# Kernel optimization log

Measured on AMD Instinct MI355X. Metric: run time of the kernel, lower is better.

The kernel has to match this reference:

```python
import jax, jax.numpy as jnp
import numpy as np

FP8_E4M3_MAX = 448.0  # max finite value of float8_e4m3fn
SCALE = 2.0           # hardcoded activation scale in FP8QDQLinear.__init__
WEIGHT_SCALE = 2.0    # hardcoded weight scale


def quantize_fp8(x, scale):
    # torchao quantize_affine_float8: divide by scale, saturate to fp8 range, cast
    return jnp.clip(x / scale, -FP8_E4M3_MAX, FP8_E4M3_MAX).astype(jnp.float8_e4m3fn)


def dequantize_fp8(q, scale):
    # torchao dequantize_affine_float8: upcast to fp32 then multiply by scale
    return q.astype(jnp.float32) * scale


def setup_inputs() -> dict:
    key = jax.random.key(0)
    k1, k2, k3 = jax.random.split(key, 3)
    in_features, out_features = 4096, 4096
    inp = jax.random.normal(k1, (4, 4096, in_features), dtype=jnp.float32)
    # weight is created as randn().to(float8_e4m3fn) in __init__ (a buffer, not a Parameter)
    weight = jax.random.normal(k2, (out_features, in_features), dtype=jnp.float32).astype(jnp.float8_e4m3fn)
    bias = jax.random.normal(k3, (out_features,), dtype=jnp.float32)
    return {"input": inp, "weight": weight, "bias": bias}


def reference(input, weight, bias):
    # dequantize fp8 weight
    w = dequantize_fp8(weight, WEIGHT_SCALE)            # [O, I] fp32
    # QDQ fake-quant on activations
    dq_input = dequantize_fp8(quantize_fp8(input, SCALE), SCALE)  # [B, S, I]
    # standard linear: y = x @ W^T + b
    out = jnp.einsum('bsi,oi->bso', dq_input, w) + bias
    return out
```

## Files before the change

### kernel.cpp

```cpp
#include <hip/hip_runtime.h>

typedef float f32x4 __attribute__((ext_vector_type(4)));
typedef float f32x16 __attribute__((ext_vector_type(16)));
typedef int i32x4 __attribute__((ext_vector_type(4)));
typedef int i32x8 __attribute__((ext_vector_type(8)));

#define M_DIM 16384L
#define N_DIM 4096L
#define K_DIM 4096L

__device__ __forceinline__ unsigned int f32_to_e4m3(float x, float scale) {
  float v = fminf(fmaxf(x * scale, -448.f), 448.f);
  unsigned int u = __float_as_uint(v);
  unsigned int s = (u >> 24) & 0x80u;
  float ax = fabsf(v);
  unsigned int ua = __float_as_uint(ax);
  unsigned int subn = (unsigned int)rintf(ax * 512.0f);
  unsigned int r = ua + 0x7FFFFu + ((ua >> 20) & 1u);
  unsigned int nrm = ((r >> 20) & 0x7FFu) - 960u;
  unsigned int mag = (ax < 0.015625f) ? subn : nrm;
  return mag | s;
}

__device__ __forceinline__ unsigned int pack4_e4m3(float4 v, float scale) {
  return f32_to_e4m3(v.x, scale) | (f32_to_e4m3(v.y, scale) << 8) |
         (f32_to_e4m3(v.z, scale) << 16) | (f32_to_e4m3(v.w, scale) << 24);
}

__global__ __launch_bounds__(256) void quant_fp8(const float* __restrict__ in,
                                                 unsigned int* __restrict__ out,
                                                 float scale) {
  const long i = (long)blockIdx.x * 256 + threadIdx.x;
  out[i] = pack4_e4m3(reinterpret_cast<const float4*>(in)[i], scale);
}

__device__ __forceinline__ void gld_lds16(const unsigned char* g, unsigned char* l) {
  __builtin_amdgcn_global_load_lds(
      (const __attribute__((address_space(1))) unsigned int*)g,
      (__attribute__((address_space(3))) unsigned int*)l,
      16, 0, 0);
}

__device__ __forceinline__ uint4 quant16(const float* p, float scale) {
  const float4* q = reinterpret_cast<const float4*>(p);
  uint4 r;
  r.x = pack4_e4m3(q[0], scale);
  r.y = pack4_e4m3(q[1], scale);
  r.z = pack4_e4m3(q[2], scale);
  r.w = pack4_e4m3(q[3], scale);
  return r;
}

__device__ __forceinline__ i32x8 ldfrag(const unsigned char* p, int p_lo) {
  i32x4 lo = *reinterpret_cast<const i32x4*>(p + p_lo * 16);
  i32x4 hi = *reinterpret_cast<const i32x4*>(p + (p_lo ^ 1) * 16);
  return i32x8{lo[0], lo[1], lo[2], lo[3], hi[0], hi[1], hi[2], hi[3]};
}

#define MFMA_SC(a, b, c) \
  __builtin_amdgcn_mfma_scale_f32_32x32x64_f8f6f4((a), (b), (c), 0, 0, 0, 0x7F7F7F7F, 0, 0x7F7F7F7F)

#define BARRIER() asm volatile("s_barrier" ::: "memory")

__global__ __launch_bounds__(256, 3) void gemm_fp8_128(
    const unsigned char* __restrict__ A8, const unsigned char* __restrict__ B8,
    const float* __restrict__ bias, float* __restrict__ C) {
  __shared__ unsigned char sA[3 * 8192];
  __shared__ unsigned char sB[3 * 8192];

  const int t = threadIdx.x;
  const int lane = t & 63;
  const int w = t >> 6;
  const int wm = w >> 1;
  const int wn = w & 1;
  const long bx = blockIdx.x;
  const long by = blockIdx.y;

  f32x16 acc[2][2] = {};

  const int l0 = t;
  const int l1 = t + 256;
  const int r0 = l0 >> 2, c0 = (l0 & 3) ^ ((l0 >> 3) & 3);
  const int r1 = l1 >> 2, c1 = (l1 & 3) ^ ((l1 >> 3) & 3);

  const unsigned char* gA0 = A8 + (by * 128 + r0) * K_DIM + c0 * 16 + 128;
  const unsigned char* gA1 = A8 + (by * 128 + r1) * K_DIM + c1 * 16 + 128;
  const unsigned char* gB0 = B8 + (bx * 128 + r0) * K_DIM + c0 * 16 + 128;
  const unsigned char* gB1 = B8 + (bx * 128 + r1) * K_DIM + c1 * 16 + 128;
  const int wofs = w * 1024;

  const int r32 = lane & 31;
  const int key = (lane >> 1) & 3;
  const int p_lo = ((lane >> 5) << 1) ^ key;

  gld_lds16(gA0 - 128, sA + wofs);
  gld_lds16(gA1 - 128, sA + 4096 + wofs);
  gld_lds16(gB0 - 128, sB + wofs);
  gld_lds16(gB1 - 128, sB + 4096 + wofs);
  gld_lds16(gA0 - 64, sA + 8192 + wofs);
  gld_lds16(gA1 - 64, sA + 8192 + 4096 + wofs);
  gld_lds16(gB0 - 64, sB + 8192 + wofs);
  gld_lds16(gB1 - 64, sB + 8192 + 4096 + wofs);
  asm volatile("s_waitcnt vmcnt(4)" ::: "memory");
  BARRIER();

  int b = 0;
  for (int kt = 0; kt < 64; ++kt) {
    int b2 = b + 2;
    if (b2 >= 3) b2 -= 3;
    const bool st = kt < 62;

    if (st) {
      unsigned char* dA = sA + b2 * 8192 + wofs;
      unsigned char* dB = sB + b2 * 8192 + wofs;
      gld_lds16(gA0, dA);
      gld_lds16(gA1, dA + 4096);
      gld_lds16(gB0, dB);
      gld_lds16(gB1, dB + 4096);
      gA0 += 64; gA1 += 64; gB0 += 64; gB1 += 64;
    }

    const unsigned char* sAw = sA + b * 8192 + wm * 4096;
    const unsigned char* sBw = sB + b * 8192 + wn * 4096;
    i32x8 af0 = ldfrag(sAw + r32 * 64, p_lo);
    i32x8 bf0 = ldfrag(sBw + r32 * 64, p_lo);
    i32x8 af1 = ldfrag(sAw + (32 + r32) * 64, p_lo);
    i32x8 bf1 = ldfrag(sBw + (32 + r32) * 64, p_lo);

    __builtin_amdgcn_s_setprio(1);
    acc[0][0] = MFMA_SC(af0, bf0, acc[0][0]);
    acc[0][1] = MFMA_SC(af0, bf1, acc[0][1]);
    acc[1][0] = MFMA_SC(af1, bf0, acc[1][0]);
    acc[1][1] = MFMA_SC(af1, bf1, acc[1][1]);
    __builtin_amdgcn_s_setprio(0);

    if (st) {
      asm volatile("s_waitcnt vmcnt(4)" ::: "memory");
    } else {
      asm volatile("s_waitcnt vmcnt(0)" ::: "memory");
    }
    BARRIER();

    if (++b == 3) b = 0;
  }

  const int mrow = 4 * (lane >> 5);
  const long gm_base = by * 128 + wm * 64;
  const long gn_base = bx * 128 + wn * 64 + r32;
#pragma unroll
  for (int nj = 0; nj < 2; ++nj) {
    const long gn = gn_base + nj * 32;
    const float bv = bias[gn];
#pragma unroll
    for (int mi = 0; mi < 2; ++mi) {
#pragma unroll
      for (int r = 0; r < 16; ++r) {
        const long gm = gm_base + mi * 32 + (r & 3) + 8 * (r >> 2) + mrow;
        C[gm * N_DIM + gn] = acc[mi][nj][r] * 4.0f + bv;
      }
    }
  }
}

template <bool FA, bool FB>
__global__ __launch_bounds__(256) void gemm_fp8_fb(const unsigned char* __restrict__ A8,
                                                   const float* __restrict__ Af,
                                                   const unsigned char* __restrict__ B8,
                                                   const float* __restrict__ Bf,
                                                   const float* __restrict__ bias,
                                                   float* __restrict__ C) {
  __shared__ unsigned char sA[128 * 64];
  __shared__ unsigned char sB[128 * 64];

  const int t = threadIdx.x;
  const int lane = t & 63;
  const int w = t >> 6;
  const int wm = w >> 1;
  const int wn = w & 1;
  const long bx = blockIdx.x;
  const long by = blockIdx.y;

  f32x16 acc[2][2] = {};

  const int l0 = w * 64 + lane;
  const int l1 = l0 + 256;
  const int r0 = l0 >> 2, c0 = (l0 & 3) ^ ((l0 >> 3) & 3);
  const int r1 = l1 >> 2, c1 = (l1 & 3) ^ ((l1 >> 3) & 3);

  const unsigned char* gA0 = nullptr; const unsigned char* gA1 = nullptr;
  const float* fA0 = nullptr;         const float* fA1 = nullptr;
  if constexpr (FA) {
    fA0 = Af + (by * 128 + r0) * K_DIM + c0 * 16;
    fA1 = Af + (by * 128 + r1) * K_DIM + c1 * 16;
  } else {
    gA0 = A8 + (by * 128 + r0) * K_DIM + c0 * 16;
    gA1 = A8 + (by * 128 + r1) * K_DIM + c1 * 16;
  }
  const unsigned char* gB0 = nullptr; const unsigned char* gB1 = nullptr;
  const float* fB0 = nullptr;         const float* fB1 = nullptr;
  if constexpr (FB) {
    fB0 = Bf + (bx * 128 + r0) * K_DIM + c0 * 16;
    fB1 = Bf + (bx * 128 + r1) * K_DIM + c1 * 16;
  } else {
    gB0 = B8 + (bx * 128 + r0) * K_DIM + c0 * 16;
    gB1 = B8 + (bx * 128 + r1) * K_DIM + c1 * 16;
  }

  unsigned char* lA0 = sA + w * 1024;
  unsigned char* lA1 = sA + 4096 + w * 1024;
  unsigned char* lB0 = sB + w * 1024;
  unsigned char* lB1 = sB + 4096 + w * 1024;

  const int r32 = lane & 31;
  const int key = (lane >> 1) & 3;
  const int p_lo = ((lane >> 5) << 1) ^ key;
  const unsigned char* sAw = sA + wm * 4096;
  const unsigned char* sBw = sB + wn * 4096;

  for (int kt = 0; kt < (int)(K_DIM / 64); ++kt) {
    if constexpr (FA) {
      *reinterpret_cast<uint4*>(sA + l0 * 16) = quant16(fA0, 0.5f);
      *reinterpret_cast<uint4*>(sA + l1 * 16) = quant16(fA1, 0.5f);
      fA0 += 64; fA1 += 64;
    } else {
      gld_lds16(gA0, lA0);
      gld_lds16(gA1, lA1);
      gA0 += 64; gA1 += 64;
    }
    if constexpr (FB) {
      *reinterpret_cast<uint4*>(sB + l0 * 16) = quant16(fB0, 1.0f);
      *reinterpret_cast<uint4*>(sB + l1 * 16) = quant16(fB1, 1.0f);
      fB0 += 64; fB1 += 64;
    } else {
      gld_lds16(gB0, lB0);
      gld_lds16(gB1, lB1);
      gB0 += 64; gB1 += 64;
    }
    __syncthreads();

    i32x8 af[2], bf[2];
#pragma unroll
    for (int i = 0; i < 2; ++i) {
      af[i] = ldfrag(sAw + (i * 32 + r32) * 64, p_lo);
      bf[i] = ldfrag(sBw + (i * 32 + r32) * 64, p_lo);
    }

#pragma unroll
    for (int i = 0; i < 2; ++i) {
#pragma unroll
      for (int j = 0; j < 2; ++j) {
        acc[i][j] = MFMA_SC(af[i], bf[j], acc[i][j]);
      }
    }
    __syncthreads();
  }

  const int mrow = 4 * (lane >> 5);
  const long gm_base = by * 128 + wm * 64;
  const long gn_base = bx * 128 + wn * 64 + r32;
#pragma unroll
  for (int nj = 0; nj < 2; ++nj) {
    const long gn = gn_base + nj * 32;
    const float bv = bias[gn];
#pragma unroll
    for (int mi = 0; mi < 2; ++mi) {
#pragma unroll
      for (int r = 0; r < 16; ++r) {
        const long gm = gm_base + mi * 32 + (r & 3) + 8 * (r >> 2) + mrow;
        C[gm * N_DIM + gn] = acc[mi][nj][r] * 4.0f + bv;
      }
    }
  }
}

extern "C" void kernel_launch(void* const* d_in, const int* in_sizes, int n_in,
                              void* d_out, int out_size, void* d_ws, size_t ws_size,
                              hipStream_t stream) {
  const float* inp = (const float*)d_in[0];
  const float* wgt = (const float*)d_in[1];
  const float* bias = (const float*)d_in[2];
  float* out = (float*)d_out;

  const size_t A_BYTES = (size_t)(M_DIM * K_DIM);
  const size_t B_BYTES = (size_t)(N_DIM * K_DIM);

  if (ws_size >= A_BYTES + B_BYTES) {
    unsigned char* aq = (unsigned char*)d_ws;
    unsigned char* wq = (unsigned char*)d_ws + A_BYTES;
    quant_fp8<<<dim3((unsigned)(M_DIM * K_DIM / 1024)), dim3(256), 0, stream>>>(
        inp, (unsigned int*)aq, 0.5f);
    quant_fp8<<<dim3((unsigned)(N_DIM * K_DIM / 1024)), dim3(256), 0, stream>>>(
        wgt, (unsigned int*)wq, 1.0f);
    gemm_fp8_128<<<dim3((unsigned)(N_DIM / 128), (unsigned)(M_DIM / 128)),
                   dim3(256), 0, stream>>>(aq, wq, bias, out);
  } else if (ws_size >= B_BYTES) {
    unsigned char* wq = (unsigned char*)d_ws;
    quant_fp8<<<dim3((unsigned)(N_DIM * K_DIM / 1024)), dim3(256), 0, stream>>>(
        wgt, (unsigned int*)wq, 1.0f);
    gemm_fp8_fb<true, false><<<dim3((unsigned)(N_DIM / 128), (unsigned)(M_DIM / 128)),
                               dim3(256), 0, stream>>>(nullptr, inp, wq, nullptr, bias, out);
  } else {
    gemm_fp8_fb<true, true><<<dim3((unsigned)(N_DIM / 128), (unsigned)(M_DIM / 128)),
                              dim3(256), 0, stream>>>(nullptr, inp, nullptr, wgt, bias, out);
  }
}
```

Baseline: 785.2 us.

## Replace triple-buffered K=64 pipeline with single-buffer K=128 tiles and 4 blocks/SM

The main fp8 GEMM drops its 3-stage LDS ring buffer of 64-wide K tiles and instead loads a single 128x128 tile per operand each iteration. Each iteration then issues two MFMA rounds and uses __syncthreads around the load/compute phases, with an 8-way XOR swizzle on the wider rows. Launch bounds rise to 4 blocks per CU so that occupancy, rather than in-block prefetch, hides global memory latency. The trade-off is that loads are no longer overlapped with compute inside a block, and the loads are waited on implicitly through the barrier.

```diff
diff --git a/kernel.cpp b/kernel.cpp
--- a/kernel.cpp
+++ b/kernel.cpp
@@ -51,22 +51,21 @@
   return r;
 }
 
-__device__ __forceinline__ i32x8 ldfrag(const unsigned char* p, int p_lo) {
+__device__ __forceinline__ i32x8 ldfrag2(const unsigned char* p, int p_lo, int ldr) {
   i32x4 lo = *reinterpret_cast<const i32x4*>(p + p_lo * 16);
   i32x4 hi = *reinterpret_cast<const i32x4*>(p + (p_lo ^ 1) * 16);
+  (void)ldr;
   return i32x8{lo[0], lo[1], lo[2], lo[3], hi[0], hi[1], hi[2], hi[3]};
 }
 
 #define MFMA_SC(a, b, c) \
   __builtin_amdgcn_mfma_scale_f32_32x32x64_f8f6f4((a), (b), (c), 0, 0, 0, 0x7F7F7F7F, 0, 0x7F7F7F7F)
 
-#define BARRIER() asm volatile("s_barrier" ::: "memory")
-
-__global__ __launch_bounds__(256, 3) void gemm_fp8_128(
+__global__ __launch_bounds__(256, 4) void gemm_fp8_128(
     const unsigned char* __restrict__ A8, const unsigned char* __restrict__ B8,
     const float* __restrict__ bias, float* __restrict__ C) {
-  __shared__ unsigned char sA[3 * 8192];
-  __shared__ unsigned char sB[3 * 8192];
+  __shared__ unsigned char sA[128 * 128];
+  __shared__ unsigned char sB[128 * 128];
 
   const int t = threadIdx.x;
   const int lane = t & 63;
@@ -78,70 +77,50 @@
 
   f32x16 acc[2][2] = {};
 
-  const int l0 = t;
-  const int l1 = t + 256;
-  const int r0 = l0 >> 2, c0 = (l0 & 3) ^ ((l0 >> 3) & 3);
-  const int r1 = l1 >> 2, c1 = (l1 & 3) ^ ((l1 >> 3) & 3);
-
-  const unsigned char* gA0 = A8 + (by * 128 + r0) * K_DIM + c0 * 16 + 128;
-  const unsigned char* gA1 = A8 + (by * 128 + r1) * K_DIM + c1 * 16 + 128;
-  const unsigned char* gB0 = B8 + (bx * 128 + r0) * K_DIM + c0 * 16 + 128;
-  const unsigned char* gB1 = B8 + (bx * 128 + r1) * K_DIM + c1 * 16 + 128;
+  const int srow = t >> 3;
+  const int sc = (t & 7) ^ ((t >> 3) & 7);
+  const unsigned char* gA0 = A8 + (by * 128 + srow) * K_DIM + sc * 16;
+  const unsigned char* gB0 = B8 + (bx * 128 + srow) * K_DIM + sc * 16;
+  const long rstep = 32 * K_DIM;
   const int wofs = w * 1024;
 
   const int r32 = lane & 31;
-  const int key = (lane >> 1) & 3;
-  const int p_lo = ((lane >> 5) << 1) ^ key;
-
-  gld_lds16(gA0 - 128, sA + wofs);
-  gld_lds16(gA1 - 128, sA + 4096 + wofs);
-  gld_lds16(gB0 - 128, sB + wofs);
-  gld_lds16(gB1 - 128, sB + 4096 + wofs);
-  gld_lds16(gA0 - 64, sA + 8192 + wofs);
-  gld_lds16(gA1 - 64, sA + 8192 + 4096 + wofs);
-  gld_lds16(gB0 - 64, sB + 8192 + wofs);
-  gld_lds16(gB1 - 64, sB + 8192 + 4096 + wofs);
-  asm volatile("s_waitcnt vmcnt(4)" ::: "memory");
-  BARRIER();
-
-  int b = 0;
-  for (int kt = 0; kt < 64; ++kt) {
-    int b2 = b + 2;
-    if (b2 >= 3) b2 -= 3;
-    const bool st = kt < 62;
-
-    if (st) {
-      unsigned char* dA = sA + b2 * 8192 + wofs;
-      unsigned char* dB = sB + b2 * 8192 + wofs;
-      gld_lds16(gA0, dA);
-      gld_lds16(gA1, dA + 4096);
-      gld_lds16(gB0, dB);
-      gld_lds16(gB1, dB + 4096);
-      gA0 += 64; gA1 += 64; gB0 += 64; gB1 += 64;
-    }
-
-    const unsigned char* sAw = sA + b * 8192 + wm * 4096;
-    const unsigned char* sBw = sB + b * 8192 + wn * 4096;
-    i32x8 af0 = ldfrag(sAw + r32 * 64, p_lo);
-    i32x8 bf0 = ldfrag(sBw + r32 * 64, p_lo);
-    i32x8 af1 = ldfrag(sAw + (32 + r32) * 64, p_lo);
-    i32x8 bf1 = ldfrag(sBw + (32 + r32) * 64, p_lo);
+  const int key = r32 & 7;
+  const int g2 = (lane >> 5) << 1;
+  const int p0 = g2 ^ key;
+  const int p1 = (4 + g2) ^ key;
+  const unsigned char* sAw = sA + (wm * 64 + r32) * 128;
+  const unsigned char* sBw = sB + (wn * 64 + r32) * 128;
+
+  for (int kt = 0; kt < (int)(K_DIM / 128); ++kt) {
+    const long ko = (long)kt * 128;
+#pragma unroll
+    for (int j = 0; j < 4; ++j) {
+      gld_lds16(gA0 + j * rstep + ko, sA + wofs + j * 4096);
+      gld_lds16(gB0 + j * rstep + ko, sB + wofs + j * 4096);
+    }
+    __syncthreads();
+
+    i32x8 af0 = ldfrag2(sAw, p0, 0);
+    i32x8 af1 = ldfrag2(sAw + 32 * 128, p0, 0);
+    i32x8 bf0 = ldfrag2(sBw, p0, 0);
+    i32x8 bf1 = ldfrag2(sBw + 32 * 128, p0, 0);
+    i32x8 af2 = ldfrag2(sAw, p1, 0);
+    i32x8 af3 = ldfrag2(sAw + 32 * 128, p1, 0);
+    i32x8 bf2 = ldfrag2(sBw, p1, 0);
+    i32x8 bf3 = ldfrag2(sBw + 32 * 128, p1, 0);
 
     __builtin_amdgcn_s_setprio(1);
     acc[0][0] = MFMA_SC(af0, bf0, acc[0][0]);
     acc[0][1] = MFMA_SC(af0, bf1, acc[0][1]);
     acc[1][0] = MFMA_SC(af1, bf0, acc[1][0]);
     acc[1][1] = MFMA_SC(af1, bf1, acc[1][1]);
+    acc[0][0] = MFMA_SC(af2, bf2, acc[0][0]);
+    acc[0][1] = MFMA_SC(af2, bf3, acc[0][1]);
+    acc[1][0] = MFMA_SC(af3, bf2, acc[1][0]);
+    acc[1][1] = MFMA_SC(af3, bf3, acc[1][1]);
     __builtin_amdgcn_s_setprio(0);
-
-    if (st) {
-      asm volatile("s_waitcnt vmcnt(4)" ::: "memory");
-    } else {
-      asm volatile("s_waitcnt vmcnt(0)" ::: "memory");
-    }
-    BARRIER();
-
-    if (++b == 3) b = 0;
+    __syncthreads();
   }
 
   const int mrow = 4 * (lane >> 5);
@@ -241,8 +220,12 @@
     i32x8 af[2], bf[2];
 #pragma unroll
     for (int i = 0; i < 2; ++i) {
-      af[i] = ldfrag(sAw + (i * 32 + r32) * 64, p_lo);
-      bf[i] = ldfrag(sBw + (i * 32 + r32) * 64, p_lo);
+      i32x4 alo = *reinterpret_cast<const i32x4*>(sAw + (i * 32 + r32) * 64 + p_lo * 16);
+      i32x4 ahi = *reinterpret_cast<const i32x4*>(sAw + (i * 32 + r32) * 64 + (p_lo ^ 1) * 16);
+      af[i] = i32x8{alo[0], alo[1], alo[2], alo[3], ahi[0], ahi[1], ahi[2], ahi[3]};
+      i32x4 blo = *reinterpret_cast<const i32x4*>(sBw + (i * 32 + r32) * 64 + p_lo * 16);
+      i32x4 bhi = *reinterpret_cast<const i32x4*>(sBw + (i * 32 + r32) * 64 + (p_lo ^ 1) * 16);
+      bf[i] = i32x8{blo[0], blo[1], blo[2], blo[3], bhi[0], bhi[1], bhi[2], bhi[3]};
     }
 
 #pragma unroll
```

After: 2.392 ms. 3.05x slower.
